# Kernel tuning notes

Measured on AMD Instinct MI355X. Metric: run time of the kernel, lower is better.

## Reference

```python
import jax, jax.numpy as jnp
import numpy as np

B, T, N, H = 512, 128, 256, 256  # batch, time_step, input_size, hidden_size


def setup_inputs() -> dict:
    key = jax.random.key(0)
    ks = jax.random.split(key, 8)
    s_lin = 1.0 / np.sqrt(T)
    s_ih = 1.0 / np.sqrt(H)
    return {
        "X": jax.random.normal(ks[0], (B, T, N), dtype=jnp.float32),
        "Wq": jax.random.uniform(ks[1], (T, T), jnp.float32, -s_lin, s_lin),
        "Wk": jax.random.uniform(ks[2], (T, T), jnp.float32, -s_lin, s_lin),
        "Wv": jax.random.uniform(ks[3], (T, T), jnp.float32, -s_lin, s_lin),
        "W_ih": jax.random.uniform(ks[4], (4 * H, N), jnp.float32, -s_ih, s_ih),
        "W_hh": jax.random.uniform(ks[5], (4 * H, H), jnp.float32, -s_ih, s_ih),
        "b_ih": jax.random.uniform(ks[6], (4 * H,), jnp.float32, -s_ih, s_ih),
        "b_hh": jax.random.uniform(ks[7], (4 * H,), jnp.float32, -s_ih, s_ih),
    }


def _forward(X, Wq, Wk, Wv, W_ih, W_hh, b_ih, b_hh):
    b, t, n = X.shape
    Xp = jnp.swapaxes(X, 1, 2)  # (B, N, T)
    Q = Xp @ Wq.T               # (B, N, T)
    K = Xp @ Wk.T               # (B, N, T)
    V = Xp @ Wv.T               # (B, N, T)
    # QK[b,i,j] = sum_t Q[b,i,t] * K[b,j,t]; scale by sqrt(N)
    scores = jnp.einsum('bit,bjt->bij', Q, K) / jnp.sqrt(jnp.float32(n))
    A = jax.nn.softmax(scores, axis=-1)          # (B, N, N)
    Xa = jnp.einsum('bij,bjt->bit', A, V)        # (B, N, T)
    Xa = jnp.swapaxes(Xa, 1, 2)                  # (B, T, N)

    h0 = jnp.zeros((b, W_hh.shape[1]), X.dtype)
    c0 = h0

    def step(carry, x_t):
        h, c = carry
        gates = x_t @ W_ih.T + b_ih + h @ W_hh.T + b_hh  # (B, 4H)
        i, f, g, o = jnp.split(gates, 4, axis=-1)         # PyTorch gate order
        i = jax.nn.sigmoid(i)
        f = jax.nn.sigmoid(f)
        g = jnp.tanh(g)
        o = jax.nn.sigmoid(o)
        c = f * c + i * g
        h = o * jnp.tanh(c)
        return (h, c), h

    _, hs = jax.lax.scan(step, (h0, c0), jnp.swapaxes(Xa, 0, 1))  # (T, B, H)
    return jnp.swapaxes(hs, 0, 1)  # (B, T, H)


def reference(X, Wq, Wk, Wv, W_ih, W_hh, b_ih, b_hh):
    return _forward(X, Wq, Wk, Wv, W_ih, W_hh, b_ih, b_hh)
```

## Files before the change

### kernel.cpp

```cpp
#include <hip/hip_runtime.h>
#include <hip/hip_bf16.h>
#include <stdint.h>


#define DI __device__ __forceinline__

typedef __attribute__((ext_vector_type(8))) short bf16x8;
typedef __attribute__((ext_vector_type(4))) short short4v;
typedef __attribute__((ext_vector_type(4))) float f32x4;
typedef __attribute__((ext_vector_type(4))) int int4v;

union U8 { bf16x8 v; short4v h[2]; int4v i; };

DI unsigned short f2bf(float x){
  union { float f; unsigned u; } v; v.f = x;
  unsigned r = v.u + 0x7fffu + ((v.u >> 16) & 1u);
  return (unsigned short)(r >> 16);
}
DI float bf2f(unsigned short x){
  union { unsigned u; float f; } v; v.u = ((unsigned)x) << 16; return v.f;
}
DI float rcp_(float x){ return __builtin_amdgcn_rcpf(x); }
DI float sigm(float x){ return rcp_(1.0f + __expf(-x)); }
DI float tanhf_(float x){ return 1.0f - 2.0f * rcp_(1.0f + __expf(2.0f * x)); }

#define BB 512
#define TT 128
#define NN 256
#define HH 256

__global__ void k_prep(const float* __restrict__ Wq, const float* __restrict__ Wk,
                       const float* __restrict__ Wv,
                       const float* __restrict__ bih, const float* __restrict__ bhh,
                       unsigned short* __restrict__ wqb, unsigned short* __restrict__ wkb,
                       unsigned short* __restrict__ wvb,
                       float* __restrict__ bias, int* __restrict__ flags){
  int i = blockIdx.x * 256 + threadIdx.x;
  if (i < 16384){ wqb[i] = f2bf(Wq[i]); wkb[i] = f2bf(Wk[i]); wvb[i] = f2bf(Wv[i]); }
  if (i < 1024){ bias[i] = bih[i] + bhh[i]; }
  if (i < 256){ flags[i] = 0; }
}

__global__ void k_prep2(const float* __restrict__ W, unsigned short* __restrict__ w_f){
  int idx = blockIdx.x * 256 + threadIdx.x;
  int j = idx >> 3, kk = idx & 7;
  const float* src = W + j * 256 + kk * 32;
  unsigned short o[32];
  #pragma unroll
  for (int g = 0; g < 4; ++g)
    #pragma unroll
    for (int e = 0; e < 4; ++e){
      o[g * 8 + e]     = f2bf(src[4 * g + e]);
      o[g * 8 + 4 + e] = f2bf(src[16 + 4 * g + e]);
    }
  int4v* dst = (int4v*)((char*)w_f + j * 512 + kk * 64);
  #pragma unroll
  for (int q = 0; q < 4; ++q) dst[q] = *(int4v*)(o + q * 8);
}

__global__ __launch_bounds__(256) void k_xpose(const float* __restrict__ X,
                                               unsigned short* __restrict__ Xp){
  __shared__ float tile[128][65];
  int b = blockIdx.y, n0 = blockIdx.x * 64;
  int tid = threadIdx.x;
  int nloc = tid & 63, t0 = tid >> 6;
  const float* src = X + (size_t)b * TT * NN + n0 + nloc;
  #pragma unroll
  for (int r = 0; r < 32; ++r){
    int t = r * 4 + t0;
    tile[t][nloc] = src[(size_t)t * NN];
  }
  __syncthreads();
  int tl = tid & 127, nr0 = tid >> 7;
  unsigned short* dst = Xp + ((size_t)b * NN + n0) * TT + tl;
  #pragma unroll
  for (int r = 0; r < 32; ++r){
    int n = r * 2 + nr0;
    dst[(size_t)n * TT] = f2bf(tile[tl][n]);
  }
}

__global__ __launch_bounds__(256) void k_qkv(const unsigned short* __restrict__ Xp,
      const unsigned short* __restrict__ Wqb, const unsigned short* __restrict__ Wkb,
      const unsigned short* __restrict__ Wvb,
      unsigned short* __restrict__ Qo, unsigned short* __restrict__ Ko,
      unsigned short* __restrict__ Vo){
  __shared__ __align__(16) char smem[32768 + 8192];
  unsigned short* Bs = (unsigned short*)smem;
  char* As = smem + 32768;
  char* Os = smem;
  int mode = blockIdx.y;
  const unsigned short* W = (mode == 0) ? Wqb : ((mode == 1) ? Wkb : Wvb);
  int m0 = blockIdx.x * 128;
  int tid = threadIdx.x;

  #pragma unroll
  for (int it = 0; it < 16; ++it){
    int c = it * 256 + tid;
    int j = c >> 5;
    int kc = (c & 31) << 2;
    short4v v = *(const short4v*)(W + j * 128 + kc);
    *(short4v*)((char*)Bs + j * 256 + ((kc * 2) ^ ((j & 7) << 4))) = v;
  }

  int lane = tid & 63, wv = tid >> 6;
  int wr = wv >> 1, wc = wv & 1;
  int l15 = lane & 15, g = lane >> 4;
  f32x4 zro = {0.f, 0.f, 0.f, 0.f};
  f32x4 acc[4][4];
  #pragma unroll
  for (int a = 0; a < 4; ++a)
    #pragma unroll
    for (int bq = 0; bq < 4; ++bq) acc[a][bq] = zro;

  int arow = tid >> 1, ahalf = (tid & 1) * 16;
  const unsigned short* Ap = Xp + (size_t)(m0 + arow) * 128;

  for (int ks = 0; ks < 4; ++ks){
    __syncthreads();
    {
      const unsigned short* s = Ap + ks * 32 + ahalf;
      char* base = As + arow * 64;
      int kb = ahalf * 2;
      int sw = (arow & 7) << 3;
      *(short4v*)(base + ((kb     ) ^ sw)) = *(const short4v*)(s);
      *(short4v*)(base + ((kb +  8) ^ sw)) = *(const short4v*)(s + 4);
      *(short4v*)(base + ((kb + 16) ^ sw)) = *(const short4v*)(s + 8);
      *(short4v*)(base + ((kb + 24) ^ sw)) = *(const short4v*)(s + 12);
    }
    __syncthreads();
    U8 af[4];
    #pragma unroll
    for (int mt = 0; mt < 4; ++mt){
      int ar = wr * 64 + mt * 16 + l15;
      const char* ab = As + ar * 64;
      int sw = (ar & 7) << 3;
      af[mt].h[0] = *(const short4v*)(ab + ((8 * g) ^ sw));
      af[mt].h[1] = *(const short4v*)(ab + ((8 * g + 32) ^ sw));
    }
    #pragma unroll
    for (int nt = 0; nt < 4; ++nt){
      int jr = wc * 64 + nt * 16 + l15;
      const char* bb = (const char*)Bs + jr * 256;
      int kb = ks * 64 + 8 * g, sw = (jr & 7) << 4;
      U8 bf;
      bf.h[0] = *(const short4v*)(bb + (kb ^ sw));
      bf.h[1] = *(const short4v*)(bb + ((kb + 32) ^ sw));
      #pragma unroll
      for (int mt = 0; mt < 4; ++mt)
        acc[mt][nt] = __builtin_amdgcn_mfma_f32_16x16x32_bf16(af[mt].v, bf.v, acc[mt][nt], 0, 0, 0);
    }
  }
  __syncthreads();
  float scale = (mode == 0) ? 0.0625f : 1.0f;
  #pragma unroll
  for (int mt = 0; mt < 4; ++mt)
    #pragma unroll
    for (int nt = 0; nt < 4; ++nt)
      #pragma unroll
      for (int r = 0; r < 4; ++r){
        int row = wr * 64 + mt * 16 + g * 4 + r;
        int col = wc * 64 + nt * 16 + l15;
        unsigned short hv = f2bf(acc[mt][nt][r] * scale);
        int addr = (mode == 2) ? (col * 256 + ((row * 2) ^ ((col & 7) << 4)))
                               : (row * 256 + ((col * 2) ^ ((row & 7) << 4)));
        *(unsigned short*)(Os + addr) = hv;
      }
  __syncthreads();
  int orow = tid >> 1, oseg = tid & 1;
  const char* srcrow = Os + orow * 256;
  unsigned short* dst;
  if (mode == 2){
    int bq = m0 >> 8, ibase = m0 & 255;
    dst = Vo + ((size_t)bq * 128 + orow) * 256 + ibase + oseg * 64;
  } else {
    dst = ((mode == 0) ? Qo : Ko) + (size_t)(m0 + orow) * 128 + oseg * 64;
  }
  #pragma unroll
  for (int c = 0; c < 8; ++c){
    int kb = oseg * 128 + c * 16;
    *(int4v*)((char*)dst + c * 16) = *(const int4v*)(srcrow + (kb ^ ((orow & 7) << 4)));
  }
}

__global__ __launch_bounds__(256) void k_attn(const unsigned short* __restrict__ Q,
        const unsigned short* __restrict__ K, const unsigned short* __restrict__ Vt,
        unsigned short* __restrict__ Xa){
  __shared__ __align__(16) char smem[16384 + 65536 + 32768 + 256];
  char* Qs = smem;
  char* Ks = smem + 16384;
  char* Ps = smem + 16384 + 65536;
  float* rden = (float*)(smem + 16384 + 65536 + 32768);
  int b = blockIdx.y, i0 = blockIdx.x * 64;
  int tid = threadIdx.x, lane = tid & 63, wv = tid >> 6;
  int l15 = lane & 15, g = lane >> 4;

  {
    int row = tid >> 2, q = tid & 3;
    const char* src = (const char*)(Q + ((size_t)b * 256 + i0 + row) * 128) + q * 64;
    char* dstr = Qs + row * 256;
    int sw = (row & 7) << 4;
    #pragma unroll
    for (int c = 0; c < 4; ++c){
      int kb = q * 64 + c * 16;
      *(int4v*)(dstr + (kb ^ sw)) = *(const int4v*)(src + c * 16);
    }
  }
  {
    const char* src = (const char*)(K + ((size_t)b * 256 + tid) * 128);
    char* dstr = Ks + tid * 256;
    int sw = (tid & 7) << 4;
    #pragma unroll
    for (int c = 0; c < 16; ++c)
      *(int4v*)(dstr + ((c * 16) ^ sw)) = *(const int4v*)(src + c * 16);
  }
  __syncthreads();

  f32x4 zro = {0.f, 0.f, 0.f, 0.f};
  f32x4 acc[16];
  #pragma unroll
  for (int nt = 0; nt < 16; ++nt) acc[nt] = zro;
  #pragma unroll
  for (int kk = 0; kk < 4; ++kk){
    int ar = wv * 16 + l15;
    const char* ab = Qs + ar * 256;
    int kb = kk * 64 + 8 * g, swa = (ar & 7) << 4;
    U8 a;
    a.h[0] = *(const short4v*)(ab + (kb ^ swa));
    a.h[1] = *(const short4v*)(ab + ((kb + 32) ^ swa));
    #pragma unroll
    for (int nt = 0; nt < 16; ++nt){
      int jr = nt * 16 + l15;
      const char* bb = Ks + jr * 256;
      int swb = (jr & 7) << 4;
      U8 bf;
      bf.h[0] = *(const short4v*)(bb + (kb ^ swb));
      bf.h[1] = *(const short4v*)(bb + ((kb + 32) ^ swb));
      acc[nt] = __builtin_amdgcn_mfma_f32_16x16x32_bf16(a.v, bf.v, acc[nt], 0, 0, 0);
    }
  }
  float mx[4], sm[4];
  #pragma unroll
  for (int r = 0; r < 4; ++r){
    float m = acc[0][r];
    #pragma unroll
    for (int nt = 1; nt < 16; ++nt) m = fmaxf(m, acc[nt][r]);
    #pragma unroll
    for (int s = 1; s < 16; s <<= 1) m = fmaxf(m, __shfl_xor(m, s));
    mx[r] = m;
  }
  #pragma unroll
  for (int r = 0; r < 4; ++r){
    float s = 0.f;
    #pragma unroll
    for (int nt = 0; nt < 16; ++nt){
      float p = __expf(acc[nt][r] - mx[r]);
      acc[nt][r] = p; s += p;
    }
    #pragma unroll
    for (int sd = 1; sd < 16; sd <<= 1) s += __shfl_xor(s, sd);
    sm[r] = s;
  }
  #pragma unroll
  for (int nt = 0; nt < 16; ++nt)
    #pragma unroll
    for (int r = 0; r < 4; ++r){
      int ir = wv * 16 + g * 4 + r;
      *(unsigned short*)(Ps + ir * 512 + ((nt * 16 + l15) * 2 ^ ((ir & 7) << 4))) = f2bf(acc[nt][r]);
    }
  #pragma unroll
  for (int r = 0; r < 4; ++r)
    if (l15 == r) rden[wv * 16 + g * 4 + r] = rcp_(sm[r]);
  __syncthreads();
  {
    int row = tid >> 1, half = tid & 1;
    const char* src = (const char*)(Vt + ((size_t)b * 128 + row) * 256) + half * 256;
    char* dstr = Ks + row * 512;
    int sw = (row & 7) << 4;
    #pragma unroll
    for (int c = 0; c < 16; ++c){
      int jb = half * 256 + c * 16;
      *(int4v*)(dstr + (jb ^ sw)) = *(const int4v*)(src + c * 16);
    }
  }
  __syncthreads();

  f32x4 acc2[2][4];
  #pragma unroll
  for (int mt = 0; mt < 2; ++mt)
    #pragma unroll
    for (int nt = 0; nt < 4; ++nt) acc2[mt][nt] = zro;
  #pragma unroll
  for (int kk = 0; kk < 8; ++kk){
    int kb = kk * 64 + 8 * g;
    U8 bfr[4];
    #pragma unroll
    for (int nt = 0; nt < 4; ++nt){
      int ir = nt * 16 + l15;
      const char* pb = Ps + ir * 512;
      int sw = (ir & 7) << 4;
      bfr[nt].h[0] = *(const short4v*)(pb + (kb ^ sw));
      bfr[nt].h[1] = *(const short4v*)(pb + ((kb + 32) ^ sw));
    }
    #pragma unroll
    for (int mt = 0; mt < 2; ++mt){
      int tr = wv * 32 + mt * 16 + l15;
      const char* ab = Ks + tr * 512;
      int sw = (tr & 7) << 4;
      U8 a;
      a.h[0] = *(const short4v*)(ab + (kb ^ sw));
      a.h[1] = *(const short4v*)(ab + ((kb + 32) ^ sw));
      #pragma unroll
      for (int nt = 0; nt < 4; ++nt)
        acc2[mt][nt] = __builtin_amdgcn_mfma_f32_16x16x32_bf16(a.v, bfr[nt].v, acc2[mt][nt], 0, 0, 0);
    }
  }
  #pragma unroll
  for (int nt = 0; nt < 4; ++nt){
    float rd = rden[nt * 16 + l15];
    #pragma unroll
    for (int mt = 0; mt < 2; ++mt)
      #pragma unroll
      for (int r = 0; r < 4; ++r){
        int t = wv * 32 + mt * 16 + g * 4 + r;
        int i = i0 + nt * 16 + l15;
        Xa[((size_t)b * 128 + t) * 256 + i] = f2bf(acc2[mt][nt][r] * rd);
      }
  }
}

__global__ __launch_bounds__(512, 2) void k_lstm8(const unsigned short* __restrict__ Xa,
        const unsigned short* __restrict__ whh_f, const unsigned short* __restrict__ wih_f,
        const float* __restrict__ bias, float* __restrict__ out,
        unsigned int* __restrict__ hbuf, int* __restrict__ flags){
  __shared__ __align__(16) char smem[131072 + 8192 + 8192 + 8448];
  char* WI = smem;
  char* HS = smem + 131072;
  char* XS = smem + 139264;
  float* GS = (float*)(smem + 147456);
  int tid = threadIdx.x, lane = tid & 63, wv = tid >> 6;
  int l15 = lane & 15, g = lane >> 4;
  int bid = blockIdx.x;
  int x = bid & 7, q = bid >> 3;
  int y = q >> 2, m = q & 3;
  int grp = y * 8 + x;
  int b0 = grp * 8;
  int c0 = m * 64;
  int tb = tid >> 6, tc = tid & 63;

  U8 breg[2][8];
  #pragma unroll
  for (int nt = 0; nt < 2; ++nt){
    int jl = wv * 32 + nt * 16 + l15;
    int jg = (jl >> 6) * 256 + c0 + (jl & 63);
    #pragma unroll
    for (int kk = 0; kk < 8; ++kk)
      breg[nt][kk].i = *(const int4v*)((const char*)whh_f + (size_t)jg * 512 + kk * 64 + g * 16);
  }
  {
    int jl = tid >> 1, hq = (tid & 1) * 16;
    int jg = (jl >> 6) * 256 + c0 + (jl & 63);
    const char* src = (const char*)wih_f + (size_t)jg * 512;
    char* dst = WI + jl * 512;
    int sx = jl & 7;
    #pragma unroll
    for (int c2 = 0; c2 < 16; ++c2){
      int c = hq + c2;
      *(int4v*)(dst + ((c ^ sx) << 4)) = *(const int4v*)(src + c * 16);
    }
  }
  { int4v z = {0,0,0,0}; *(int4v*)(HS + tid * 16) = z; }
  if (tid < 256){ int4v z = {0,0,0,0}; *(int4v*)(XS + 4096 + tid * 16) = z; }
  {
    short4v v = *(const short4v*)(Xa + ((size_t)(b0 + tb) * 128) * 256 + tc * 4);
    *(short4v*)(XS + tb * 512 + ((tc * 8) ^ ((tb & 7) << 3))) = v;
  }
  float bs0 = bias[      c0 + tc], bs1 = bias[256 + c0 + tc];
  float bs2 = bias[512 + c0 + tc], bs3 = bias[768 + c0 + tc];
  float cst = 0.f;
  __syncthreads();

  int swA = (l15 & 7) << 3;
  const char* hsrow = HS + l15 * 512;
  const char* xsrow = XS + l15 * 512;
  const char* wib0 = WI + (wv * 32 + l15) * 512;
  const char* wib1 = WI + (wv * 32 + 16 + l15) * 512;
  int keep = g >> 1;
  f32x4 zro = {0.f, 0.f, 0.f, 0.f};

  f32x4 accX[2] = {zro, zro};
  #pragma unroll
  for (int kk = 0; kk < 8; ++kk){
    U8 a2, w0, w1;
    a2.h[0] = *(const short4v*)(xsrow + ((kk * 64 + 8 * g) ^ swA));
    a2.h[1] = *(const short4v*)(xsrow + ((kk * 64 + 32 + 8 * g) ^ swA));
    int cx = ((kk * 4 + g) ^ (l15 & 7)) << 4;
    w0.i = *(const int4v*)(wib0 + cx);
    w1.i = *(const int4v*)(wib1 + cx);
    accX[0] = __builtin_amdgcn_mfma_f32_16x16x32_bf16(a2.v, w0.v, accX[0], 0, 0, 0);
    accX[1] = __builtin_amdgcn_mfma_f32_16x16x32_bf16(a2.v, w1.v, accX[1], 0, 0, 0);
  }

  #pragma unroll 1
  for (int t = 0; t < 128; ++t){
    short4v xan = {0, 0, 0, 0};
    if (t < 127)
      xan = *(const short4v*)(Xa + ((size_t)(b0 + tb) * 128 + (t + 1)) * 256 + tc * 4);
    f32x4 acc[2] = {accX[0], accX[1]};
    #pragma unroll
    for (int kk = 0; kk < 8; ++kk){
      U8 a;
      a.h[0] = *(const short4v*)(hsrow + ((kk * 64 + 8 * g) ^ swA));
      a.h[1] = *(const short4v*)(hsrow + ((kk * 64 + 32 + 8 * g) ^ swA));
      acc[0] = __builtin_amdgcn_mfma_f32_16x16x32_bf16(a.v, breg[0][kk].v, acc[0], 0, 0, 0);
      acc[1] = __builtin_amdgcn_mfma_f32_16x16x32_bf16(a.v, breg[1][kk].v, acc[1], 0, 0, 0);
    }
    #pragma unroll
    for (int r = 0; r < 4; ++r){
      float v0 = acc[0][r], v1 = acc[1][r];
      float kv = keep ? v1 : v0;
      float sv = keep ? v0 : v1;
      float val = kv + __shfl_xor(sv, 32);
      int jl = wv * 32 + keep * 16 + l15;
      int batch = (g & 1) * 4 + r;
      GS[batch * 264 + (jl >> 6) * 66 + (jl & 63)] = val;
    }
    __syncthreads();
    float gv0 = GS[tb * 264 +   0 + tc];
    float gv1 = GS[tb * 264 +  66 + tc];
    float gv2 = GS[tb * 264 + 132 + tc];
    float gv3 = GS[tb * 264 + 198 + tc];
    float gi = sigm(gv0 + bs0);
    float gf = sigm(gv1 + bs1);
    float gg = tanhf_(gv2 + bs2);
    float go = sigm(gv3 + bs3);
    float c = gf * cst + gi * gg;
    cst = c;
    float h = go * tanhf_(c);
    out[((size_t)(b0 + tb) * 128 + t) * 256 + c0 + tc] = h;
    if (t < 127){
      unsigned short hhi = f2bf(h);
      unsigned short hlo = f2bf(h - bf2f(hhi));
      unsigned int pk = (unsigned int)hhi | ((unsigned int)hlo << 16);
      unsigned int* hb = hbuf + ((size_t)grp * 2 + (t & 1)) * 2048;
      __hip_atomic_store(hb + tb * 256 + c0 + tc, pk, __ATOMIC_RELAXED, __HIP_MEMORY_SCOPE_SYSTEM);
      *(short4v*)(XS + tb * 512 + ((tc * 8) ^ ((tb & 7) << 3))) = xan;
      __syncthreads();
      if (wv == 0 && lane == 0)
        __hip_atomic_store(&flags[grp * 4 + m], t + 1, __ATOMIC_RELAXED, __HIP_MEMORY_SCOPE_SYSTEM);
      accX[0] = zro; accX[1] = zro;
      #pragma unroll
      for (int kk = 0; kk < 8; ++kk){
        U8 a2, w0, w1;
        a2.h[0] = *(const short4v*)(xsrow + ((kk * 64 + 8 * g) ^ swA));
        a2.h[1] = *(const short4v*)(xsrow + ((kk * 64 + 32 + 8 * g) ^ swA));
        int cx = ((kk * 4 + g) ^ (l15 & 7)) << 4;
        w0.i = *(const int4v*)(wib0 + cx);
        w1.i = *(const int4v*)(wib1 + cx);
        accX[0] = __builtin_amdgcn_mfma_f32_16x16x32_bf16(a2.v, w0.v, accX[0], 0, 0, 0);
        accX[1] = __builtin_amdgcn_mfma_f32_16x16x32_bf16(a2.v, w1.v, accX[1], 0, 0, 0);
      }
      if (wv == 0 && lane >= 1 && lane <= 3){
        int pl = lane - 1;
        int pslot = pl + (pl >= m ? 1 : 0);
        while (__hip_atomic_load(&flags[grp * 4 + pslot], __ATOMIC_RELAXED,
                                 __HIP_MEMORY_SCOPE_SYSTEM) <= t){}
      }
      __syncthreads();
      {
        int bb = tid >> 6, cg = tid & 63;
        const unsigned long long* sp =
            (const unsigned long long*)(hb + bb * 256 + cg * 4);
        unsigned long long w0 = __hip_atomic_load(sp,     __ATOMIC_RELAXED, __HIP_MEMORY_SCOPE_SYSTEM);
        unsigned long long w1 = __hip_atomic_load(sp + 1, __ATOMIC_RELAXED, __HIP_MEMORY_SCOPE_SYSTEM);
        unsigned int u0 = (unsigned int)w0, u1 = (unsigned int)(w0 >> 32);
        unsigned int u2 = (unsigned int)w1, u3 = (unsigned int)(w1 >> 32);
        short4v hiv = { (short)(u0 & 0xffff), (short)(u1 & 0xffff),
                        (short)(u2 & 0xffff), (short)(u3 & 0xffff) };
        short4v lov = { (short)(u0 >> 16), (short)(u1 >> 16),
                        (short)(u2 >> 16), (short)(u3 >> 16) };
        int sw = (bb & 7) << 3;
        int cb = (cg * 8) ^ sw;
        *(short4v*)(HS + bb * 512 + cb) = hiv;
        *(short4v*)(HS + (bb + 8) * 512 + cb) = lov;
      }
      __syncthreads();
    }
  }
}

extern "C" void kernel_launch(void* const* d_in, const int* in_sizes, int n_in,
                              void* d_out, int out_size, void* d_ws, size_t ws_size,
                              hipStream_t stream){
  (void)in_sizes; (void)n_in; (void)out_size; (void)ws_size;
  const float* X   = (const float*)d_in[0];
  const float* Wq  = (const float*)d_in[1];
  const float* Wk  = (const float*)d_in[2];
  const float* Wv  = (const float*)d_in[3];
  const float* Wih = (const float*)d_in[4];
  const float* Whh = (const float*)d_in[5];
  const float* bih = (const float*)d_in[6];
  const float* bhh = (const float*)d_in[7];
  float* out = (float*)d_out;
  char* ws = (char*)d_ws;

  const size_t SZ = 33554432ULL;
  unsigned short* p_xp = (unsigned short*)ws;
  unsigned short* p_q  = (unsigned short*)(ws + SZ);
  unsigned short* p_k  = (unsigned short*)(ws + 2 * SZ);
  unsigned short* p_vt = (unsigned short*)(ws + 3 * SZ);
  unsigned short* p_xa = (unsigned short*)(ws + 4 * SZ);
  char* p = ws + 5 * SZ;
  unsigned short* p_wqb = (unsigned short*)p; p += 32768;
  unsigned short* p_wkb = (unsigned short*)p; p += 32768;
  unsigned short* p_wvb = (unsigned short*)p; p += 32768;
  unsigned short* p_whhf= (unsigned short*)p; p += 524288;
  unsigned short* p_wihf= (unsigned short*)p; p += 524288;
  float* p_bias = (float*)p; p += 4096;
  unsigned int* p_hbuf = (unsigned int*)p; p += 1048576;
  int* p_flags = (int*)p;

  k_prep<<<64, 256, 0, stream>>>(Wq, Wk, Wv, bih, bhh,
                                 p_wqb, p_wkb, p_wvb, p_bias, p_flags);
  k_prep2<<<32, 256, 0, stream>>>(Whh, p_whhf);
  k_prep2<<<32, 256, 0, stream>>>(Wih, p_wihf);
  k_xpose<<<dim3(4, 512), 256, 0, stream>>>(X, p_xp);
  k_qkv<<<dim3(1024, 3), 256, 0, stream>>>(p_xp, p_wqb, p_wkb, p_wvb, p_q, p_k, p_vt);
  k_attn<<<dim3(4, 512), 256, 0, stream>>>(p_q, p_k, p_vt, p_xa);
  k_lstm8<<<256, 512, 0, stream>>>(p_xa, p_whhf, p_wihf, p_bias, out, p_hbuf, p_flags);
}
```

Measured before the change: 528.2 us.

## Fuse X transpose into QKV projection and widen attention blocks

The separate transpose kernel is folded into the QKV kernel, which now loads a 128-column fp32 slice of X, transposes and converts it to bf16 in shared memory, and computes Q, K and V in one block by looping over the three weight matrices. This removes the round trip of the transposed bf16 X through global memory and one kernel launch, and reuses the staged X tile for all three projections. The attention kernel now handles 128 query rows per block with 512 threads and reuses shared memory for P and V, which halves the number of times K and V are reloaded per batch. The cost is much larger shared memory per block, which lowers occupancy, and fewer total blocks.

```diff
diff --git a/kernel.cpp b/kernel.cpp
--- a/kernel.cpp
+++ b/kernel.cpp
@@ -58,140 +58,134 @@
   for (int q = 0; q < 4; ++q) dst[q] = *(int4v*)(o + q * 8);
 }
 
-__global__ __launch_bounds__(256) void k_xpose(const float* __restrict__ X,
-                                               unsigned short* __restrict__ Xp){
-  __shared__ float tile[128][65];
-  int b = blockIdx.y, n0 = blockIdx.x * 64;
-  int tid = threadIdx.x;
-  int nloc = tid & 63, t0 = tid >> 6;
-  const float* src = X + (size_t)b * TT * NN + n0 + nloc;
-  #pragma unroll
-  for (int r = 0; r < 32; ++r){
-    int t = r * 4 + t0;
-    tile[t][nloc] = src[(size_t)t * NN];
-  }
-  __syncthreads();
-  int tl = tid & 127, nr0 = tid >> 7;
-  unsigned short* dst = Xp + ((size_t)b * NN + n0) * TT + tl;
-  #pragma unroll
-  for (int r = 0; r < 32; ++r){
-    int n = r * 2 + nr0;
-    dst[(size_t)n * TT] = f2bf(tile[tl][n]);
-  }
-}
-
-__global__ __launch_bounds__(256) void k_qkv(const unsigned short* __restrict__ Xp,
+__global__ __launch_bounds__(256) void k_qkv2(const float* __restrict__ X,
       const unsigned short* __restrict__ Wqb, const unsigned short* __restrict__ Wkb,
       const unsigned short* __restrict__ Wvb,
       unsigned short* __restrict__ Qo, unsigned short* __restrict__ Ko,
       unsigned short* __restrict__ Vo){
-  __shared__ __align__(16) char smem[32768 + 8192];
-  unsigned short* Bs = (unsigned short*)smem;
-  char* As = smem + 32768;
-  char* Os = smem;
-  int mode = blockIdx.y;
-  const unsigned short* W = (mode == 0) ? Wqb : ((mode == 1) ? Wkb : Wvb);
-  int m0 = blockIdx.x * 128;
+  __shared__ __align__(16) char smem[98816];
+  char* As2 = smem;
+  float* tile = (float*)(smem + 32768);
+  char* Bs = smem + 32768;
+  char* Os = smem + 65536;
+  int bid = blockIdx.x;
+  int b = bid >> 1, nh = bid & 1;
+  int n0 = nh * 128;
+  int m0 = b * 256 + n0;
   int tid = threadIdx.x;
 
-  #pragma unroll
-  for (int it = 0; it < 16; ++it){
-    int c = it * 256 + tid;
-    int j = c >> 5;
-    int kc = (c & 31) << 2;
-    short4v v = *(const short4v*)(W + j * 128 + kc);
-    *(short4v*)((char*)Bs + j * 256 + ((kc * 2) ^ ((j & 7) << 4))) = v;
+  {
+    int nl = tid & 127, tg = tid >> 7;
+    const float* src = X + (size_t)b * TT * NN + n0 + nl;
+    #pragma unroll
+    for (int r = 0; r < 64; ++r){
+      int t = r * 2 + tg;
+      tile[t * 129 + nl] = src[(size_t)t * NN];
+    }
+  }
+  __syncthreads();
+  {
+    int tpos = tid & 31, nrow = tid >> 5;
+    #pragma unroll
+    for (int rr = 0; rr < 16; ++rr){
+      int n = rr * 8 + nrow;
+      int t0 = tpos * 4;
+      short4v v = { (short)f2bf(tile[(t0    ) * 129 + n]),
+                    (short)f2bf(tile[(t0 + 1) * 129 + n]),
+                    (short)f2bf(tile[(t0 + 2) * 129 + n]),
+                    (short)f2bf(tile[(t0 + 3) * 129 + n]) };
+      *(short4v*)(As2 + n * 256 + ((t0 * 2) ^ ((n & 7) << 4))) = v;
+    }
   }
 
   int lane = tid & 63, wv = tid >> 6;
   int wr = wv >> 1, wc = wv & 1;
   int l15 = lane & 15, g = lane >> 4;
   f32x4 zro = {0.f, 0.f, 0.f, 0.f};
-  f32x4 acc[4][4];
-  #pragma unroll
-  for (int a = 0; a < 4; ++a)
-    #pragma unroll
-    for (int bq = 0; bq < 4; ++bq) acc[a][bq] = zro;
-
-  int arow = tid >> 1, ahalf = (tid & 1) * 16;
-  const unsigned short* Ap = Xp + (size_t)(m0 + arow) * 128;
-
-  for (int ks = 0; ks < 4; ++ks){
+
+  #pragma unroll 1
+  for (int mode = 0; mode < 3; ++mode){
+    const unsigned short* W = (mode == 0) ? Wqb : ((mode == 1) ? Wkb : Wvb);
     __syncthreads();
-    {
-      const unsigned short* s = Ap + ks * 32 + ahalf;
-      char* base = As + arow * 64;
-      int kb = ahalf * 2;
-      int sw = (arow & 7) << 3;
-      *(short4v*)(base + ((kb     ) ^ sw)) = *(const short4v*)(s);
-      *(short4v*)(base + ((kb +  8) ^ sw)) = *(const short4v*)(s + 4);
-      *(short4v*)(base + ((kb + 16) ^ sw)) = *(const short4v*)(s + 8);
-      *(short4v*)(base + ((kb + 24) ^ sw)) = *(const short4v*)(s + 12);
+    #pragma unroll
+    for (int it = 0; it < 16; ++it){
+      int c = it * 256 + tid;
+      int j = c >> 5;
+      int kc = (c & 31) << 2;
+      short4v v = *(const short4v*)(W + j * 128 + kc);
+      *(short4v*)(Bs + j * 256 + ((kc * 2) ^ ((j & 7) << 4))) = v;
     }
     __syncthreads();
-    U8 af[4];
-    #pragma unroll
-    for (int mt = 0; mt < 4; ++mt){
-      int ar = wr * 64 + mt * 16 + l15;
-      const char* ab = As + ar * 64;
-      int sw = (ar & 7) << 3;
-      af[mt].h[0] = *(const short4v*)(ab + ((8 * g) ^ sw));
-      af[mt].h[1] = *(const short4v*)(ab + ((8 * g + 32) ^ sw));
-    }
-    #pragma unroll
-    for (int nt = 0; nt < 4; ++nt){
-      int jr = wc * 64 + nt * 16 + l15;
-      const char* bb = (const char*)Bs + jr * 256;
-      int kb = ks * 64 + 8 * g, sw = (jr & 7) << 4;
-      U8 bf;
-      bf.h[0] = *(const short4v*)(bb + (kb ^ sw));
-      bf.h[1] = *(const short4v*)(bb + ((kb + 32) ^ sw));
+    f32x4 acc[4][4];
+    #pragma unroll
+    for (int a = 0; a < 4; ++a)
       #pragma unroll
-      for (int mt = 0; mt < 4; ++mt)
-        acc[mt][nt] = __builtin_amdgcn_mfma_f32_16x16x32_bf16(af[mt].v, bf.v, acc[mt][nt], 0, 0, 0);
-    }
-  }
-  __syncthreads();
-  float scale = (mode == 0) ? 0.0625f : 1.0f;
-  #pragma unroll
-  for (int mt = 0; mt < 4; ++mt)
-    #pragma unroll
-    for (int nt = 0; nt < 4; ++nt)
+      for (int bq = 0; bq < 4; ++bq) acc[a][bq] = zro;
+    #pragma unroll
+    for (int ks = 0; ks < 4; ++ks){
+      U8 af[4];
       #pragma unroll
-      for (int r = 0; r < 4; ++r){
-        int row = wr * 64 + mt * 16 + g * 4 + r;
-        int col = wc * 64 + nt * 16 + l15;
-        unsigned short hv = f2bf(acc[mt][nt][r] * scale);
-        int addr = (mode == 2) ? (col * 256 + ((row * 2) ^ ((col & 7) << 4)))
-                               : (row * 256 + ((col * 2) ^ ((row & 7) << 4)));
-        *(unsigned short*)(Os + addr) = hv;
+      for (int mt = 0; mt < 4; ++mt){
+        int ar = wr * 64 + mt * 16 + l15;
+        const char* ab = As2 + ar * 256;
+        int sw = (ar & 7) << 4;
+        af[mt].h[0] = *(const short4v*)(ab + ((ks * 64 + 8 * g) ^ sw));
+        af[mt].h[1] = *(const short4v*)(ab + ((ks * 64 + 8 * g + 32) ^ sw));
       }
-  __syncthreads();
-  int orow = tid >> 1, oseg = tid & 1;
-  const char* srcrow = Os + orow * 256;
-  unsigned short* dst;
-  if (mode == 2){
-    int bq = m0 >> 8, ibase = m0 & 255;
-    dst = Vo + ((size_t)bq * 128 + orow) * 256 + ibase + oseg * 64;
-  } else {
-    dst = ((mode == 0) ? Qo : Ko) + (size_t)(m0 + orow) * 128 + oseg * 64;
-  }
-  #pragma unroll
-  for (int c = 0; c < 8; ++c){
-    int kb = oseg * 128 + c * 16;
-    *(int4v*)((char*)dst + c * 16) = *(const int4v*)(srcrow + (kb ^ ((orow & 7) << 4)));
-  }
-}
-
-__global__ __launch_bounds__(256) void k_attn(const unsigned short* __restrict__ Q,
+      #pragma unroll
+      for (int nt = 0; nt < 4; ++nt){
+        int jr = wc * 64 + nt * 16 + l15;
+        const char* bb = Bs + jr * 256;
+        int kb = ks * 64 + 8 * g, sw = (jr & 7) << 4;
+        U8 bf;
+        bf.h[0] = *(const short4v*)(bb + (kb ^ sw));
+        bf.h[1] = *(const short4v*)(bb + ((kb + 32) ^ sw));
+        #pragma unroll
+        for (int mt = 0; mt < 4; ++mt)
+          acc[mt][nt] = __builtin_amdgcn_mfma_f32_16x16x32_bf16(af[mt].v, bf.v, acc[mt][nt], 0, 0, 0);
+      }
+    }
+    float scale = (mode == 0) ? 0.0625f : 1.0f;
+    #pragma unroll
+    for (int mt = 0; mt < 4; ++mt)
+      #pragma unroll
+      for (int nt = 0; nt < 4; ++nt)
+        #pragma unroll
+        for (int r = 0; r < 4; ++r){
+          int row = wr * 64 + mt * 16 + g * 4 + r;
+          int col = wc * 64 + nt * 16 + l15;
+          unsigned short hv = f2bf(acc[mt][nt][r] * scale);
+          int addr = (mode == 2) ? (col * 256 + ((row * 2) ^ ((col & 7) << 4)))
+                                 : (row * 256 + ((col * 2) ^ ((row & 7) << 4)));
+          *(unsigned short*)(Os + addr) = hv;
+        }
+    __syncthreads();
+    int orow = tid >> 1, oseg = tid & 1;
+    const char* srcrow = Os + orow * 256;
+    unsigned short* dst;
+    if (mode == 2){
+      dst = Vo + ((size_t)b * 128 + orow) * 256 + n0 + oseg * 64;
+    } else {
+      dst = ((mode == 0) ? Qo : Ko) + (size_t)(m0 + orow) * 128 + oseg * 64;
+    }
+    #pragma unroll
+    for (int c = 0; c < 8; ++c){
+      int kb = oseg * 128 + c * 16;
+      *(int4v*)((char*)dst + c * 16) = *(const int4v*)(srcrow + (kb ^ ((orow & 7) << 4)));
+    }
+  }
+}
+
+__global__ __launch_bounds__(512) void k_attn2(const unsigned short* __restrict__ Q,
         const unsigned short* __restrict__ K, const unsigned short* __restrict__ Vt,
         unsigned short* __restrict__ Xa){
-  __shared__ __align__(16) char smem[16384 + 65536 + 32768 + 256];
+  __shared__ __align__(16) char smem[131072 + 512];
   char* Qs = smem;
-  char* Ks = smem + 16384;
-  char* Ps = smem + 16384 + 65536;
-  float* rden = (float*)(smem + 16384 + 65536 + 32768);
-  int b = blockIdx.y, i0 = blockIdx.x * 64;
+  char* Ks = smem + 32768;
+  char* Ps = smem;
+  char* Vs = smem + 65536;
+  float* rden = (float*)(smem + 131072);
+  int b = blockIdx.y, i0 = blockIdx.x * 128;
   int tid = threadIdx.x, lane = tid & 63, wv = tid >> 6;
   int l15 = lane & 15, g = lane >> 4;
 
@@ -207,12 +201,15 @@
     }
   }
   {
-    const char* src = (const char*)(K + ((size_t)b * 256 + tid) * 128);
-    char* dstr = Ks + tid * 256;
-    int sw = (tid & 7) << 4;
-    #pragma unroll
-    for (int c = 0; c < 16; ++c)
-      *(int4v*)(dstr + ((c * 16) ^ sw)) = *(const int4v*)(src + c * 16);
+    int row = tid >> 1, half = tid & 1;
+    const char* src = (const char*)(K + ((size_t)b * 256 + row) * 128) + half * 128;
+    char* dstr = Ks + row * 256;
+    int sw = (row & 7) << 4;
+    #pragma unroll
+    for (int c = 0; c < 8; ++c){
+      int kb = half * 128 + c * 16;
+      *(int4v*)(dstr + (kb ^ sw)) = *(const int4v*)(src + c * 16);
+    }
   }
   __syncthreads();
 
@@ -261,6 +258,7 @@
     for (int sd = 1; sd < 16; sd <<= 1) s += __shfl_xor(s, sd);
     sm[r] = s;
   }
+  __syncthreads();
   #pragma unroll
   for (int nt = 0; nt < 16; ++nt)
     #pragma unroll
@@ -271,61 +269,53 @@
   #pragma unroll
   for (int r = 0; r < 4; ++r)
     if (l15 == r) rden[wv * 16 + g * 4 + r] = rcp_(sm[r]);
+  {
+    int row = tid >> 2, q = tid & 3;
+    const char* src = (const char*)(Vt + ((size_t)b * 128 + row) * 256) + q * 128;
+    char* dstr = Vs + row * 512;
+    int sw = (row & 7) << 4;
+    #pragma unroll
+    for (int c = 0; c < 8; ++c){
+      int jb = q * 128 + c * 16;
+      *(int4v*)(dstr + (jb ^ sw)) = *(const int4v*)(src + c * 16);
+    }
+  }
   __syncthreads();
-  {
-    int row = tid >> 1, half = tid & 1;
-    const char* src = (const char*)(Vt + ((size_t)b * 128 + row) * 256) + half * 256;
-    char* dstr = Ks + row * 512;
-    int sw = (row & 7) << 4;
-    #pragma unroll
-    for (int c = 0; c < 16; ++c){
-      int jb = half * 256 + c * 16;
-      *(int4v*)(dstr + (jb ^ sw)) = *(const int4v*)(src + c * 16);
-    }
-  }
-  __syncthreads();
-
-  f32x4 acc2[2][4];
-  #pragma unroll
-  for (int mt = 0; mt < 2; ++mt)
-    #pragma unroll
-    for (int nt = 0; nt < 4; ++nt) acc2[mt][nt] = zro;
+
+  f32x4 acc2[8];
+  #pragma unroll
+  for (int nt = 0; nt < 8; ++nt) acc2[nt] = zro;
   #pragma unroll
   for (int kk = 0; kk < 8; ++kk){
     int kb = kk * 64 + 8 * g;
-    U8 bfr[4];
-    #pragma unroll
-    for (int nt = 0; nt < 4; ++nt){
+    U8 bfr[8];
+    #pragma unroll
+    for (int nt = 0; nt < 8; ++nt){
       int ir = nt * 16 + l15;
       const char* pb = Ps + ir * 512;
       int sw = (ir & 7) << 4;
       bfr[nt].h[0] = *(const short4v*)(pb + (kb ^ sw));
       bfr[nt].h[1] = *(const short4v*)(pb + ((kb + 32) ^ sw));
     }
-    #pragma unroll
-    for (int mt = 0; mt < 2; ++mt){
-      int tr = wv * 32 + mt * 16 + l15;
-      const char* ab = Ks + tr * 512;
-      int sw = (tr & 7) << 4;
-      U8 a;
-      a.h[0] = *(const short4v*)(ab + (kb ^ sw));
-      a.h[1] = *(const short4v*)(ab + ((kb + 32) ^ sw));
-      #pragma unroll
-      for (int nt = 0; nt < 4; ++nt)
-        acc2[mt][nt] = __builtin_amdgcn_mfma_f32_16x16x32_bf16(a.v, bfr[nt].v, acc2[mt][nt], 0, 0, 0);
-    }
-  }
-  #pragma unroll
-  for (int nt = 0; nt < 4; ++nt){
+    int tr = wv * 16 + l15;
+    const char* ab = Vs + tr * 512;
+    int sw = (tr & 7) << 4;
+    U8 a;
+    a.h[0] = *(const short4v*)(ab + (kb ^ sw));
+    a.h[1] = *(const short4v*)(ab + ((kb + 32) ^ sw));
+    #pragma unroll
+    for (int nt = 0; nt < 8; ++nt)
+      acc2[nt] = __builtin_amdgcn_mfma_f32_16x16x32_bf16(a.v, bfr[nt].v, acc2[nt], 0, 0, 0);
+  }
+  #pragma unroll
+  for (int nt = 0; nt < 8; ++nt){
     float rd = rden[nt * 16 + l15];
     #pragma unroll
-    for (int mt = 0; mt < 2; ++mt)
-      #pragma unroll
-      for (int r = 0; r < 4; ++r){
-        int t = wv * 32 + mt * 16 + g * 4 + r;
-        int i = i0 + nt * 16 + l15;
-        Xa[((size_t)b * 128 + t) * 256 + i] = f2bf(acc2[mt][nt][r] * rd);
-      }
+    for (int r = 0; r < 4; ++r){
+      int t = wv * 16 + g * 4 + r;
+      int i = i0 + nt * 16 + l15;
+      Xa[((size_t)b * 128 + t) * 256 + i] = f2bf(acc2[nt][r] * rd);
+    }
   }
 }
 
@@ -505,12 +495,11 @@
   char* ws = (char*)d_ws;
 
   const size_t SZ = 33554432ULL;
-  unsigned short* p_xp = (unsigned short*)ws;
-  unsigned short* p_q  = (unsigned short*)(ws + SZ);
-  unsigned short* p_k  = (unsigned short*)(ws + 2 * SZ);
-  unsigned short* p_vt = (unsigned short*)(ws + 3 * SZ);
-  unsigned short* p_xa = (unsigned short*)(ws + 4 * SZ);
-  char* p = ws + 5 * SZ;
+  unsigned short* p_q  = (unsigned short*)ws;
+  unsigned short* p_k  = (unsigned short*)(ws + SZ);
+  unsigned short* p_vt = (unsigned short*)(ws + 2 * SZ);
+  unsigned short* p_xa = (unsigned short*)(ws + 3 * SZ);
+  char* p = ws + 4 * SZ;
   unsigned short* p_wqb = (unsigned short*)p; p += 32768;
   unsigned short* p_wkb = (unsigned short*)p; p += 32768;
   unsigned short* p_wvb = (unsigned short*)p; p += 32768;
@@ -524,8 +513,7 @@
                                  p_wqb, p_wkb, p_wvb, p_bias, p_flags);
   k_prep2<<<32, 256, 0, stream>>>(Whh, p_whhf);
   k_prep2<<<32, 256, 0, stream>>>(Wih, p_wihf);
-  k_xpose<<<dim3(4, 512), 256, 0, stream>>>(X, p_xp);
-  k_qkv<<<dim3(1024, 3), 256, 0, stream>>>(p_xp, p_wqb, p_wkb, p_wvb, p_q, p_k, p_vt);
-  k_attn<<<dim3(4, 512), 256, 0, stream>>>(p_q, p_k, p_vt, p_xa);
+  k_qkv2<<<1024, 256, 0, stream>>>(X, p_wqb, p_wkb, p_wvb, p_q, p_k, p_vt);
+  k_attn2<<<dim3(2, 512), 512, 0, stream>>>(p_q, p_k, p_vt, p_xa);
   k_lstm8<<<256, 512, 0, stream>>>(p_xa, p_whhf, p_wihf, p_bias, out, p_hbuf, p_flags);
 }
```

New measurement: 525.7 us. Within noise of the previous version (-0.5%).
